# Optimization experiments

Hardware: AMD Instinct MI355X
Metric: run time of the kernel (lower is better)

## Reference

```python
import jax, jax.numpy as jnp
import numpy as np
from jax import lax

B, L, V, D = 64, 1024, 256, 512
DROPOUT = 0.1   # embedding dropout rate
ZONEOUT = 0.1   # bernoulli prob of keeping previous state (zoneout)


def setup_inputs() -> dict:
    key = jax.random.key(0)
    ks = jax.random.split(key, 5)
    tokens = jax.random.randint(ks[0], (B, L), 0, V)
    lengths = jax.random.randint(ks[1], (B,), 1, L + 1)
    embed = jax.random.normal(ks[2], (V, D), jnp.float32) * 0.02
    s = 1.0 / np.sqrt(2 * D).astype(np.float32)
    W_fwd = jax.random.normal(ks[3], (2 * D, 4 * D), jnp.float32) * s
    b_fwd = jnp.zeros((4 * D,), jnp.float32)
    W_bwd = jax.random.normal(ks[4], (2 * D, 4 * D), jnp.float32) * s
    b_bwd = jnp.zeros((4 * D,), jnp.float32)
    return {"tokens": tokens, "lengths": lengths, "embed": embed,
            "W_fwd": W_fwd, "b_fwd": b_fwd, "W_bwd": W_bwd, "b_bwd": b_bwd}


def _lstm_scan(x_tbd, reset_tb, W, b, key):
    # x_tbd: [L, B, D] time-major inputs; reset_tb: [L, B] bool (ResetCore mask)
    Bsz = x_tbd.shape[1]
    Dh = W.shape[1] // 4
    zeros = jnp.zeros((Bsz, Dh), x_tbd.dtype)

    def step(carry, inp):
        h, c, k = carry
        x_t, r_t = inp
        # hk.ResetCore: reset state to initial (zeros) where mask is True
        h = jnp.where(r_t[:, None], 0.0, h)
        c = jnp.where(r_t[:, None], 0.0, c)
        kz, k = jax.random.split(k)
        gated = jnp.concatenate([x_t, h], axis=-1) @ W + b  # [B, 4*Dh]
        i, g, f, o = jnp.split(gated, 4, axis=-1)
        f = jax.nn.sigmoid(f + 1.0)
        c_new = f * c + jax.nn.sigmoid(i) * jnp.tanh(g)
        h_new = jax.nn.sigmoid(o) * jnp.tanh(c_new)
        # zoneout: with prob ZONEOUT keep previous hidden/cell
        zm = jax.random.bernoulli(kz, ZONEOUT, (2,) + h.shape)
        h_out = jnp.where(zm[0], h, h_new)
        c_out = jnp.where(zm[1], c, c_new)
        return (h_out, c_out, k), h_out

    _, hs = lax.scan(step, (zeros, zeros, key), (x_tbd, reset_tb))
    return hs  # [L, B, Dh]


def reference(tokens, lengths, embed, W_fwd, b_fwd, W_bwd, b_bwd):
    key = jax.random.key(42)
    kd, kf, kb = jax.random.split(key, 3)
    x = embed[tokens]  # [B, L, D]
    # embedding dropout (is_training=True)
    keep = jax.random.bernoulli(kd, 1.0 - DROPOUT, x.shape)
    x = jnp.where(keep, x / (1.0 - DROPOUT), 0.0)
    Lx = x.shape[1]
    mask = jnp.arange(Lx)[None, :] < lengths[:, None] - 1  # [B, L]
    x_t = jnp.moveaxis(x, 1, 0)  # [L, B, D] time-major
    no_reset = jnp.zeros((Lx, x.shape[0]), bool)
    h_fwd = _lstm_scan(x_t, no_reset, W_fwd, b_fwd, kf)
    # backward pass on flipped sequence with flipped reset mask (ResetCore)
    h_bwd = _lstm_scan(jnp.flip(x_t, 0), jnp.flip(mask, 1).T, W_bwd, b_bwd, kb)
    h_bwd = jnp.flip(h_bwd, 0)
    out = jnp.concatenate([h_fwd, h_bwd], axis=-1)  # [L, B, 2*D]
    return jnp.moveaxis(out, 0, 1)  # [B, L, 2*D]
```

## Files before the change

### kernel.cpp

```cpp
#include <hip/hip_runtime.h>
#include <hip/hip_bf16.h>
#include <stdint.h>

typedef unsigned short u16;
typedef unsigned int   u32;
typedef unsigned long long u64;
typedef __bf16 bf16x8 __attribute__((ext_vector_type(8)));
typedef float  f32x4  __attribute__((ext_vector_type(4)));

__device__ __forceinline__ u32 rotl32(u32 v, int d){ return (v<<d)|(v>>(32-d)); }

__device__ __forceinline__ void tf2x32(u32 k0, u32 k1, u32 c0, u32 c1, u32 &o0, u32 &o1){
  u32 ks0=k0, ks1=k1, ks2=k0^k1^0x1BD11BDAu;
  u32 x0=c0+ks0, x1=c1+ks1;
  x0+=x1; x1=rotl32(x1,13); x1^=x0;  x0+=x1; x1=rotl32(x1,15); x1^=x0;
  x0+=x1; x1=rotl32(x1,26); x1^=x0;  x0+=x1; x1=rotl32(x1, 6); x1^=x0;
  x0+=ks1; x1+=ks2+1u;
  x0+=x1; x1=rotl32(x1,17); x1^=x0;  x0+=x1; x1=rotl32(x1,29); x1^=x0;
  x0+=x1; x1=rotl32(x1,16); x1^=x0;  x0+=x1; x1=rotl32(x1,24); x1^=x0;
  x0+=ks2; x1+=ks0+2u;
  x0+=x1; x1=rotl32(x1,13); x1^=x0;  x0+=x1; x1=rotl32(x1,15); x1^=x0;
  x0+=x1; x1=rotl32(x1,26); x1^=x0;  x0+=x1; x1=rotl32(x1, 6); x1^=x0;
  x0+=ks0; x1+=ks1+3u;
  x0+=x1; x1=rotl32(x1,17); x1^=x0;  x0+=x1; x1=rotl32(x1,29); x1^=x0;
  x0+=x1; x1=rotl32(x1,16); x1^=x0;  x0+=x1; x1=rotl32(x1,24); x1^=x0;
  x0+=ks1; x1+=ks2+4u;
  x0+=x1; x1=rotl32(x1,13); x1^=x0;  x0+=x1; x1=rotl32(x1,15); x1^=x0;
  x0+=x1; x1=rotl32(x1,26); x1^=x0;  x0+=x1; x1=rotl32(x1, 6); x1^=x0;
  x0+=ks2; x1+=ks0+5u;
  o0=x0; o1=x1;
}

__device__ __forceinline__ float u01(u32 b){ return __uint_as_float((b>>9)|0x3f800000u) - 1.0f; }
__device__ __forceinline__ u16 f2bf(float v){ __hip_bfloat16 h = __float2bfloat16(v); return *reinterpret_cast<u16*>(&h); }
__device__ __forceinline__ float bf2f(u16 b){ __hip_bfloat16 h; *reinterpret_cast<u16*>(&h)=b; return __bfloat162float(h); }
__device__ __forceinline__ float sigm(float x){ return 1.0f/(1.0f + __expf(-x)); }
__device__ __forceinline__ float tanh_f(float x){ return 1.0f - 2.0f/(__expf(2.0f*x) + 1.0f); }

extern "C" __global__ void __launch_bounds__(256) prep_k(
    const float* __restrict__ Wf, const float* __restrict__ Wb,
    u16* __restrict__ wpack, u32* __restrict__ flags, u32* __restrict__ code, u32* __restrict__ keys){
  u32 gid = blockIdx.x*256u + threadIdx.x;
  if (gid < 8192u) flags[gid] = 0u;
  if (gid == 0u){
    *code = 0u;
    u32 d0,d1,f0,f1,g0,g1;
    tf2x32(0u,42u, 0u,0u, d0,d1);
    tf2x32(0u,42u, 0u,1u, f0,f1);
    tf2x32(0u,42u, 0u,2u, g0,g1);
    keys[0]=d0; keys[1]=d1; keys[2]=f0; keys[3]=f1; keys[4]=g0; keys[5]=g1;
  }
  if (gid == 1u){
    u32 r0,r1; bool ok = true;
    tf2x32(0u,0u,0u,0u,r0,r1);
    ok = ok && (r0==0x6b200159u) && (r1==0x99ba4efeu);
    tf2x32(0x13198a2eu,0x03707344u,0x243f6a88u,0x85a308d3u,r0,r1);
    ok = ok && (r0==0xc4923a9cu) && (r1==0x483df7a0u);
    tf2x32(0xffffffffu,0xffffffffu,0xffffffffu,0xffffffffu,r0,r1);
    ok = ok && (r0==0x1cb996fcu) && (r1==0xbb002be7u);
    if (!ok) __hip_atomic_fetch_or(code, 4u, __ATOMIC_RELAXED, __HIP_MEMORY_SCOPE_AGENT);
  }
  u32 idx = gid >> 6, lane = gid & 63u;
  u32 mat = idx & 3u; u32 r = idx >> 2;
  u32 gt = r & 3u; r >>= 2;
  u32 kt = r & 15u; r >>= 4;
  u32 ug = r & 31u; u32 dir = r >> 5;
  u32 col = gt*512u + ug*16u + (lane & 15u);
  u32 kb  = kt*32u + ((lane>>4)<<3);
  const float* W = dir ? Wb : Wf;
  bool hrow = (mat==1u || mat==2u);
  bool lo   = (mat==2u || mat==3u);
  u16 o[8];
  #pragma unroll
  for (int j=0;j<8;j++){
    u32 k = kb + (u32)j;
    u32 row = hrow ? (512u + k) : k;
    float v = W[(size_t)row*2048u + col];
    u16 h = f2bf(v);
    o[j] = lo ? f2bf(v - bf2f(h)) : h;
  }
  u16* dst = wpack + ((size_t)idx*64u + lane)*8u;
  uint4 pk;
  pk.x = (u32)o[0] | ((u32)o[1]<<16);
  pk.y = (u32)o[2] | ((u32)o[3]<<16);
  pk.z = (u32)o[4] | ((u32)o[5]<<16);
  pk.w = (u32)o[6] | ((u32)o[7]<<16);
  *(uint4*)dst = pk;
}

extern "C" __global__ void __launch_bounds__(256) embed_k(
    const int* __restrict__ tokens, const float* __restrict__ emb,
    const u32* __restrict__ keys, u16* __restrict__ X, u16* __restrict__ XLO, int xsplit){
  u32 gid = blockIdx.x*256u + threadIdx.x;
  u32 kd0 = keys[0], kd1 = keys[1];
  u32 i0 = gid << 1;
  u32 a0,a1,b0,b1;
  tf2x32(kd0,kd1, 0u, i0,     a0,a1);
  tf2x32(kd0,kd1, 0u, i0|1u,  b0,b1);
  u32 bb = i0 >> 19, l = (i0 >> 9) & 1023u, d = i0 & 511u;
  int tok = tokens[(bb<<10)|l];
  const float* ep = emb + (size_t)(u32)tok*512u + d;
  float e0 = ep[0], e1 = ep[1];
  float v0 = (u01(a0^a1) < 0.9f) ? (e0/0.9f) : 0.0f;
  float v1 = (u01(b0^b1) < 0.9f) ? (e1/0.9f) : 0.0f;
  size_t off = (((size_t)l<<6)|bb)*512u + d;
  u16 h0 = f2bf(v0), h1 = f2bf(v1);
  *(u32*)(X+off) = (u32)h0 | ((u32)h1<<16);
  if (xsplit){
    u16 l0 = f2bf(v0 - bf2f(h0)), l1 = f2bf(v1 - bf2f(h1));
    *(u32*)(XLO+off) = (u32)l0 | ((u32)l1<<16);
  }
}

extern "C" __global__ void __launch_bounds__(256,1) lstm_k(
    const u16* __restrict__ wpack, const u16* __restrict__ X, const u16* __restrict__ XLO,
    u32* hbuf, u32* chk, u32* flags, u32* code, const u32* __restrict__ keys,
    const int* __restrict__ lengths, const float* __restrict__ bF, const float* __restrict__ bB,
    float* __restrict__ out, int xsplit){
  __shared__ u16 xHi[16][520];
  __shared__ u16 xLoS[16][520];
  __shared__ u16 hHi[16][520];
  __shared__ u16 hLo[16][520];
  __shared__ float gparts[4][4][16][17];
  __shared__ u32 kzS[2];
  (void)chk;

  const int tid  = threadIdx.x;
  const int wid  = tid >> 6;
  const int lane = tid & 63;
  const int q    = lane >> 4, n15 = lane & 15;
  const int bx   = blockIdx.x;
  const int dir  = (bx & 7) >> 2, bg = bx & 3, ug = bx >> 3;
  const int grp  = dir*4 + bg;
  const int eb   = tid >> 4, eu = tid & 15;
  const int scol = eu * 32;

  if (bx == 0 && wid == 0){
    bf16x8 aI, aI2, bT;
    #pragma unroll
    for (int j=0;j<8;j++){
      int k = q*8 + j;
      aI[j]  = (__bf16)((k == n15)    ? 1.0f : 0.0f);
      aI2[j] = (__bf16)((k == n15+16) ? 1.0f : 0.0f);
      bT[j]  = (__bf16)((float)((k & 15)*16 + n15));
    }
    f32x4 z = {0.0f,0.0f,0.0f,0.0f};
    f32x4 d1 = __builtin_amdgcn_mfma_f32_16x16x32_bf16(aI,  bT, z, 0,0,0);
    f32x4 d2 = __builtin_amdgcn_mfma_f32_16x16x32_bf16(aI2, bT, z, 0,0,0);
    bool ok = true;
    #pragma unroll
    for (int r=0;r<4;r++){
      float ex = (float)((q*4 + r)*16 + n15);
      ok = ok && (d1[r] == ex) && (d2[r] == ex);
    }
    if (__any(ok ? 0 : 1) && lane == 0)
      __hip_atomic_fetch_or(code, 1u, __ATOMIC_RELAXED, __HIP_MEMORY_SCOPE_AGENT);
  }

  u32 kc0 = keys[2 + dir*2], kc1 = keys[3 + dir*2];

  bf16x8 BW[4][4][4];
  #pragma unroll
  for (int ktl=0;ktl<4;ktl++)
    #pragma unroll
    for (int gt=0;gt<4;gt++)
      #pragma unroll
      for (int mat=0;mat<4;mat++){
        size_t idx = ((((size_t)(dir*32+ug)*16 + (size_t)(wid*4+ktl))*4 + gt)*4 + mat);
        BW[mat][ktl][gt] = *(const bf16x8*)(wpack + (idx*64 + lane)*8);
      }

  const float* bias = dir ? bB : bF;
  float biasr[4];
  #pragma unroll
  for (int g=0;g<4;g++) biasr[g] = bias[g*512 + ug*16 + eu];
  const int lenb = lengths[bg*16 + eb];

  float cReg = 0.0f, hReg = 0.0f;

  u32* stamps = flags + grp*32;
  u32* hb_base = hbuf + (size_t)grp*2*16*512;
  const size_t outbase = (size_t)(bg*16+eb)*1048576 + (size_t)(dir*512 + ug*16 + eu);

  for (int t=0; t<1024; ++t){
    if (wid == 0){
      u32 A0,A1,B0,B1;
      tf2x32(kc0,kc1, 0u,0u, A0,A1);
      tf2x32(kc0,kc1, 0u,1u, B0,B1);
      if (lane==0){ kzS[0]=A0; kzS[1]=A1; }
      kc0=B0; kc1=B1;
    }
    const int tx = dir ? (1023 - t) : t;
    {
      size_t xoff = (((size_t)tx*64) + (size_t)(bg*16 + eb))*512 + scol;
      const uint4* xs = (const uint4*)(X + xoff);
      uint4* xd = (uint4*)&xHi[eb][scol];
      xd[0]=xs[0]; xd[1]=xs[1]; xd[2]=xs[2]; xd[3]=xs[3];
      if (xsplit){
        const uint4* ls = (const uint4*)(XLO + xoff);
        uint4* ld = (uint4*)&xLoS[eb][scol];
        ld[0]=ls[0]; ld[1]=ls[1]; ld[2]=ls[2]; ld[3]=ls[3];
      }
    }
    __syncthreads();

    const u32 cnt = (u32)((bg*16+eb)*512 + ug*16+eu);
    u32 p0,p1,q0,q1;
    tf2x32(kzS[0], kzS[1], 0u, cnt,          p0,p1);
    tf2x32(kzS[0], kzS[1], 0u, cnt+32768u,   q0,q1);
    const bool keepH = (u01(p0^p1) < 0.1f);
    const bool keepC = (u01(q0^q1) < 0.1f);

    f32x4 zz = {0.0f,0.0f,0.0f,0.0f};
    f32x4 acc[4] = {zz,zz,zz,zz};
    #pragma unroll
    for (int ktl=0;ktl<4;ktl++){
      const int ko = (wid*4+ktl)*32 + q*8;
      bf16x8 ax = *(const bf16x8*)&xHi[n15][ko];
      #pragma unroll
      for (int gt=0;gt<4;gt++){
        acc[gt] = __builtin_amdgcn_mfma_f32_16x16x32_bf16(ax, BW[0][ktl][gt], acc[gt], 0,0,0);
        acc[gt] = __builtin_amdgcn_mfma_f32_16x16x32_bf16(ax, BW[3][ktl][gt], acc[gt], 0,0,0);
      }
      if (xsplit){
        bf16x8 axl = *(const bf16x8*)&xLoS[n15][ko];
        #pragma unroll
        for (int gt=0;gt<4;gt++)
          acc[gt] = __builtin_amdgcn_mfma_f32_16x16x32_bf16(axl, BW[0][ktl][gt], acc[gt], 0,0,0);
      }
    }

    const bool rst = (dir==1) && (t > 1024 - lenb);
    if (t > 0){
      if (tid < 32){
        const u32* sp = stamps + tid;
        while (__hip_atomic_load(sp, __ATOMIC_RELAXED, __HIP_MEMORY_SCOPE_AGENT) < (u32)t) {}
      }
      __syncthreads();
    }
    if (t == 0 || rst){
      uint4 z; z.x=0u; z.y=0u; z.z=0u; z.w=0u;
      uint4* hd = (uint4*)&hHi[eb][scol];
      uint4* ld = (uint4*)&hLo[eb][scol];
      hd[0]=z;hd[1]=z;hd[2]=z;hd[3]=z;  ld[0]=z;ld[1]=z;ld[2]=z;ld[3]=z;
    } else {
      const u64* hrow64 = (const u64*)(hb_base + ((size_t)((t-1)&1)*16 + eb)*512 + scol);
      u32 hv[32];
      #pragma unroll
      for (int i=0;i<16;i++){
        u64 v = __hip_atomic_load(hrow64 + i, __ATOMIC_RELAXED, __HIP_MEMORY_SCOPE_AGENT);
        hv[2*i]   = (u32)v;
        hv[2*i+1] = (u32)(v >> 32);
      }
      u32 hiw[16], low[16];
      #pragma unroll
      for (int k=0;k<16;k++){
        hiw[k] = (hv[2*k] & 0xFFFFu) | (hv[2*k+1] << 16);
        low[k] = (hv[2*k] >> 16)     | (hv[2*k+1] & 0xFFFF0000u);
      }
      uint4* hd = (uint4*)&hHi[eb][scol];
      uint4* ld = (uint4*)&hLo[eb][scol];
      #pragma unroll
      for (int v=0;v<4;v++){
        uint4 hw; hw.x=hiw[4*v]; hw.y=hiw[4*v+1]; hw.z=hiw[4*v+2]; hw.w=hiw[4*v+3];
        uint4 lw; lw.x=low[4*v]; lw.y=low[4*v+1]; lw.z=low[4*v+2]; lw.w=low[4*v+3];
        hd[v]=hw; ld[v]=lw;
      }
    }
    __syncthreads();

    #pragma unroll
    for (int ktl=0;ktl<4;ktl++){
      const int ko = (wid*4+ktl)*32 + q*8;
      bf16x8 ahi = *(const bf16x8*)&hHi[n15][ko];
      bf16x8 alo = *(const bf16x8*)&hLo[n15][ko];
      #pragma unroll
      for (int gt=0;gt<4;gt++){
        acc[gt] = __builtin_amdgcn_mfma_f32_16x16x32_bf16(ahi, BW[1][ktl][gt], acc[gt], 0,0,0);
        acc[gt] = __builtin_amdgcn_mfma_f32_16x16x32_bf16(ahi, BW[2][ktl][gt], acc[gt], 0,0,0);
        acc[gt] = __builtin_amdgcn_mfma_f32_16x16x32_bf16(alo, BW[1][ktl][gt], acc[gt], 0,0,0);
      }
    }
    #pragma unroll
    for (int gt=0;gt<4;gt++)
      #pragma unroll
      for (int r=0;r<4;r++)
        gparts[wid][gt][q*4+r][n15] = acc[gt][r];
    __syncthreads();

    float gv[4];
    #pragma unroll
    for (int g=0;g<4;g++)
      gv[g] = gparts[0][g][eb][eu]+gparts[1][g][eb][eu]+gparts[2][g][eb][eu]+gparts[3][g][eb][eu]+biasr[g];
    float cp = cReg, hprev = hReg;
    if (rst){ cp = 0.0f; hprev = 0.0f; }
    float fg = sigm(gv[2] + 1.0f);
    float cn = fg*cp + sigm(gv[0])*tanh_f(gv[1]);
    float hn = sigm(gv[3])*tanh_f(cn);
    float ho = keepH ? hprev : hn;
    float co = keepC ? cp    : cn;
    cReg = co; hReg = ho;
    u16 hhi = f2bf(ho); u16 hlo = f2bf(ho - bf2f(hhi));
    u32 hp32 = ((u32)hlo<<16) | (u32)hhi;
    __hip_atomic_store(hb_base + ((size_t)(t&1)*16 + eb)*512 + (size_t)(ug*16+eu), hp32,
                       __ATOMIC_RELAXED, __HIP_MEMORY_SCOPE_AGENT);
    __syncthreads();
    if (tid == 0)
      __hip_atomic_store(stamps + ug, (u32)(t+1), __ATOMIC_RELAXED, __HIP_MEMORY_SCOPE_AGENT);
    out[outbase + ((size_t)tx << 10)] = ho;
  }

  if (bx == 0 && tid == 0){
    u32 c = __hip_atomic_load(code, __ATOMIC_ACQUIRE, __HIP_MEMORY_SCOPE_AGENT);
    if (c != 0u) out[0] = 1000.0f * (float)c;
  }
}

extern "C" void kernel_launch(void* const* d_in, const int* in_sizes, int n_in,
                              void* d_out, int out_size, void* d_ws, size_t ws_size,
                              hipStream_t stream) {
  const int*   tokens  = (const int*)d_in[0];
  const int*   lengths = (const int*)d_in[1];
  const float* embed   = (const float*)d_in[2];
  const float* Wf      = (const float*)d_in[3];
  const float* bF      = (const float*)d_in[4];
  const float* Wb      = (const float*)d_in[5];
  const float* bB      = (const float*)d_in[6];
  float* out = (float*)d_out;

  const size_t SZ_WPACK = 16777216ull;
  const size_t SZ_X     = 67108864ull;
  const size_t SZ_HBUF  = 524288ull;
  const size_t SZ_CHK   = 65536ull;
  const size_t SZ_FLAGS = 32768ull;
  size_t need_full = SZ_WPACK + 2*SZ_X + SZ_HBUF + SZ_CHK + SZ_FLAGS + 128;
  int xsplit = (ws_size >= need_full) ? 1 : 0;

  char* p = (char*)d_ws;
  u16* wpack = (u16*)p;            p += SZ_WPACK;
  u16* X     = (u16*)p;            p += SZ_X;
  u16* XLO   = xsplit ? (u16*)p : X;
  if (xsplit)                      p += SZ_X;
  u32* hbuf  = (u32*)p;            p += SZ_HBUF;
  u32* chk   = (u32*)p;            p += SZ_CHK;
  u32* flags = (u32*)p;            p += SZ_FLAGS;
  u32* code  = (u32*)p;            p += 64;
  u32* keys  = (u32*)p;

  prep_k<<<dim3(4096), dim3(256), 0, stream>>>(Wf, Wb, wpack, flags, code, keys);
  embed_k<<<dim3(65536), dim3(256), 0, stream>>>(tokens, embed, keys, X, XLO, xsplit);
  lstm_k<<<dim3(256), dim3(256), 0, stream>>>(wpack, X, XLO, hbuf, chk, flags, code, keys,
                                              lengths, bF, bB, out, xsplit);
}
```

Measured before the change: 8.178 ms.

## Prefetch next-step inputs via async LDS loads and pad barrier flags apart

Double-buffers the per-step x tile in shared memory and fills the next buffer with asynchronous global_load_lds while the current step computes. The inter-block wait moves to the top of the step, and the h loads are issued early into registers. Each block's stamp flag now sits in its own 128-byte slot to avoid false sharing. This roughly doubles x LDS use and relies on async-load ordering across the existing barriers.

```diff
diff --git a/kernel.cpp b/kernel.cpp
--- a/kernel.cpp
+++ b/kernel.cpp
@@ -36,6 +36,12 @@
 __device__ __forceinline__ float bf2f(u16 b){ __hip_bfloat16 h; *reinterpret_cast<u16*>(&h)=b; return __bfloat162float(h); }
 __device__ __forceinline__ float sigm(float x){ return 1.0f/(1.0f + __expf(-x)); }
 __device__ __forceinline__ float tanh_f(float x){ return 1.0f - 2.0f/(__expf(2.0f*x) + 1.0f); }
+
+__device__ __forceinline__ void gload_lds16(const u16* g, u16* l){
+  __builtin_amdgcn_global_load_lds(
+      (const __attribute__((address_space(1))) unsigned int*)g,
+      (__attribute__((address_space(3))) unsigned int*)l, 16, 0, 0);
+}
 
 extern "C" __global__ void __launch_bounds__(256) prep_k(
     const float* __restrict__ Wf, const float* __restrict__ Wb,
@@ -117,8 +123,8 @@
     u32* hbuf, u32* chk, u32* flags, u32* code, const u32* __restrict__ keys,
     const int* __restrict__ lengths, const float* __restrict__ bF, const float* __restrict__ bB,
     float* __restrict__ out, int xsplit){
-  __shared__ u16 xHi[16][520];
-  __shared__ u16 xLoS[16][520];
+  __shared__ u16 xHi[2][16][520];
+  __shared__ u16 xLoS[2][16][520];
   __shared__ u16 hHi[16][520];
   __shared__ u16 hLo[16][520];
   __shared__ float gparts[4][4][16][17];
@@ -178,11 +184,24 @@
 
   float cReg = 0.0f, hReg = 0.0f;
 
-  u32* stamps = flags + grp*32;
   u32* hb_base = hbuf + (size_t)grp*2*16*512;
   const size_t outbase = (size_t)(bg*16+eb)*1048576 + (size_t)(dir*512 + ug*16 + eu);
 
+  {
+    const int tx0 = dir ? 1023 : 0;
+    #pragma unroll
+    for (int j=0;j<4;j++){
+      const int rb = wid*4 + j;
+      const size_t go = (((size_t)tx0*64) + (size_t)(bg*16 + rb))*512 + (size_t)lane*8;
+      gload_lds16(X + go, &xHi[0][rb][0]);
+      if (xsplit) gload_lds16(XLO + go, &xLoS[0][rb][0]);
+    }
+  }
+
   for (int t=0; t<1024; ++t){
+    const int cur = t & 1, nxt = cur ^ 1;
+    const int tx = dir ? (1023 - t) : t;
+
     if (wid == 0){
       u32 A0,A1,B0,B1;
       tf2x32(kc0,kc1, 0u,0u, A0,A1);
@@ -190,20 +209,31 @@
       if (lane==0){ kzS[0]=A0; kzS[1]=A1; }
       kc0=B0; kc1=B1;
     }
-    const int tx = dir ? (1023 - t) : t;
-    {
-      size_t xoff = (((size_t)tx*64) + (size_t)(bg*16 + eb))*512 + scol;
-      const uint4* xs = (const uint4*)(X + xoff);
-      uint4* xd = (uint4*)&xHi[eb][scol];
-      xd[0]=xs[0]; xd[1]=xs[1]; xd[2]=xs[2]; xd[3]=xs[3];
-      if (xsplit){
-        const uint4* ls = (const uint4*)(XLO + xoff);
-        uint4* ld = (uint4*)&xLoS[eb][scol];
-        ld[0]=ls[0]; ld[1]=ls[1]; ld[2]=ls[2]; ld[3]=ls[3];
-      }
+    if (t > 0 && wid == 3 && lane < 32){
+      const u32* sp = flags + (((size_t)grp*32 + (u32)lane) << 5);
+      while (__hip_atomic_load(sp, __ATOMIC_RELAXED, __HIP_MEMORY_SCOPE_AGENT) < (u32)t) {}
     }
     __syncthreads();
 
+    const bool rst = (dir==1) && (t > 1024 - lenb);
+    const bool hload = (t > 0) && !rst;
+    u64 hv64[16];
+    if (hload){
+      const u64* hrow64 = (const u64*)(hb_base + ((size_t)((t-1)&1)*16 + eb)*512 + scol);
+      #pragma unroll
+      for (int i=0;i<16;i++)
+        hv64[i] = __hip_atomic_load(hrow64 + i, __ATOMIC_RELAXED, __HIP_MEMORY_SCOPE_AGENT);
+    }
+    if (t < 1023){
+      const int txn = dir ? (1022 - t) : (t + 1);
+      #pragma unroll
+      for (int j=0;j<4;j++){
+        const int rb = wid*4 + j;
+        const size_t go = (((size_t)txn*64) + (size_t)(bg*16 + rb))*512 + (size_t)lane*8;
+        gload_lds16(X + go, &xHi[nxt][rb][0]);
+        if (xsplit) gload_lds16(XLO + go, &xLoS[nxt][rb][0]);
+      }
+    }
     const u32 cnt = (u32)((bg*16+eb)*512 + ug*16+eu);
     u32 p0,p1,q0,q1;
     tf2x32(kzS[0], kzS[1], 0u, cnt,          p0,p1);
@@ -216,47 +246,32 @@
     #pragma unroll
     for (int ktl=0;ktl<4;ktl++){
       const int ko = (wid*4+ktl)*32 + q*8;
-      bf16x8 ax = *(const bf16x8*)&xHi[n15][ko];
+      bf16x8 ax = *(const bf16x8*)&xHi[cur][n15][ko];
       #pragma unroll
       for (int gt=0;gt<4;gt++){
         acc[gt] = __builtin_amdgcn_mfma_f32_16x16x32_bf16(ax, BW[0][ktl][gt], acc[gt], 0,0,0);
         acc[gt] = __builtin_amdgcn_mfma_f32_16x16x32_bf16(ax, BW[3][ktl][gt], acc[gt], 0,0,0);
       }
       if (xsplit){
-        bf16x8 axl = *(const bf16x8*)&xLoS[n15][ko];
+        bf16x8 axl = *(const bf16x8*)&xLoS[cur][n15][ko];
         #pragma unroll
         for (int gt=0;gt<4;gt++)
           acc[gt] = __builtin_amdgcn_mfma_f32_16x16x32_bf16(axl, BW[0][ktl][gt], acc[gt], 0,0,0);
       }
     }
 
-    const bool rst = (dir==1) && (t > 1024 - lenb);
-    if (t > 0){
-      if (tid < 32){
-        const u32* sp = stamps + tid;
-        while (__hip_atomic_load(sp, __ATOMIC_RELAXED, __HIP_MEMORY_SCOPE_AGENT) < (u32)t) {}
-      }
-      __syncthreads();
-    }
-    if (t == 0 || rst){
+    if (!hload){
       uint4 z; z.x=0u; z.y=0u; z.z=0u; z.w=0u;
       uint4* hd = (uint4*)&hHi[eb][scol];
       uint4* ld = (uint4*)&hLo[eb][scol];
       hd[0]=z;hd[1]=z;hd[2]=z;hd[3]=z;  ld[0]=z;ld[1]=z;ld[2]=z;ld[3]=z;
     } else {
-      const u64* hrow64 = (const u64*)(hb_base + ((size_t)((t-1)&1)*16 + eb)*512 + scol);
-      u32 hv[32];
-      #pragma unroll
-      for (int i=0;i<16;i++){
-        u64 v = __hip_atomic_load(hrow64 + i, __ATOMIC_RELAXED, __HIP_MEMORY_SCOPE_AGENT);
-        hv[2*i]   = (u32)v;
-        hv[2*i+1] = (u32)(v >> 32);
-      }
       u32 hiw[16], low[16];
       #pragma unroll
       for (int k=0;k<16;k++){
-        hiw[k] = (hv[2*k] & 0xFFFFu) | (hv[2*k+1] << 16);
-        low[k] = (hv[2*k] >> 16)     | (hv[2*k+1] & 0xFFFF0000u);
+        u32 lo32 = (u32)hv64[k], hi32 = (u32)(hv64[k] >> 32);
+        hiw[k] = (lo32 & 0xFFFFu) | (hi32 << 16);
+        low[k] = (lo32 >> 16)     | (hi32 & 0xFFFF0000u);
       }
       uint4* hd = (uint4*)&hHi[eb][scol];
       uint4* ld = (uint4*)&hLo[eb][scol];
@@ -306,7 +321,8 @@
                        __ATOMIC_RELAXED, __HIP_MEMORY_SCOPE_AGENT);
     __syncthreads();
     if (tid == 0)
-      __hip_atomic_store(stamps + ug, (u32)(t+1), __ATOMIC_RELAXED, __HIP_MEMORY_SCOPE_AGENT);
+      __hip_atomic_store(flags + (((size_t)grp*32 + ug) << 5), (u32)(t+1),
+                         __ATOMIC_RELAXED, __HIP_MEMORY_SCOPE_AGENT);
     out[outbase + ((size_t)tx << 10)] = ho;
   }
 
```

New measurement: 7.379 ms. -9.8%, faster.
